# Optimization experiments

Measured on AMD Instinct MI355X. Metric: run time of the kernel, lower is better.

Reference implementation:

```python
import jax, jax.numpy as jnp
import numpy as np

B, S, D = 2, 2048, 2048
H, KVH, HD = 8, 1, 256
N_REP = H // KVH
WIN = 1024
THETA = 10000.0
SCALE = 1.0 / (HD ** 0.5)


def setup_inputs() -> dict:
    key = jax.random.key(0)
    k1, k2, k3, k4, k5 = jax.random.split(key, 5)
    hidden_states = jax.random.normal(k1, (B, S, D), dtype=jnp.float32)
    neg = jnp.finfo(jnp.float32).min
    causal = jnp.where(jnp.tril(jnp.ones((S, S), jnp.float32)) == 1.0, 0.0, neg)
    attention_mask = jnp.broadcast_to(causal[None, None], (B, 1, S, S)).copy()
    position_ids = jnp.broadcast_to(jnp.arange(S, dtype=jnp.int32)[None, :], (B, S)).copy()
    std = 0.02
    Wq = std * jax.random.normal(k2, (H * HD, D), dtype=jnp.float32)
    Wk = std * jax.random.normal(k3, (KVH * HD, D), dtype=jnp.float32)
    Wv = std * jax.random.normal(k4, (KVH * HD, D), dtype=jnp.float32)
    Wo = std * jax.random.normal(k5, (D, H * HD), dtype=jnp.float32)
    return {"hidden_states": hidden_states, "attention_mask": attention_mask,
            "position_ids": position_ids, "Wq": Wq, "Wk": Wk, "Wv": Wv, "Wo": Wo}


def _rotate_half(x):
    x1, x2 = x[..., : HD // 2], x[..., HD // 2:]
    return jnp.concatenate([-x2, x1], axis=-1)


def _rope(position_ids):
    inv_freq = 1.0 / (THETA ** (jnp.arange(0, HD, 2, dtype=jnp.float32) / HD))  # [HD/2]
    freqs = position_ids.astype(jnp.float32)[:, :, None] * inv_freq  # [b,s,HD/2]
    emb = jnp.concatenate([freqs, freqs], axis=-1)  # [b,s,HD]
    # unsqueeze at head dim -> [b,1,s,HD]
    return jnp.cos(emb)[:, None], jnp.sin(emb)[:, None]


def reference(hidden_states, attention_mask, position_ids, Wq, Wk, Wv, Wo):
    b, s, _ = hidden_states.shape
    q = (hidden_states @ Wq.T).reshape(b, s, H, HD).transpose(0, 2, 1, 3)    # [b,H,s,hd]
    k = (hidden_states @ Wk.T).reshape(b, s, KVH, HD).transpose(0, 2, 1, 3)  # [b,KVH,s,hd]
    v = (hidden_states @ Wv.T).reshape(b, s, KVH, HD).transpose(0, 2, 1, 3)

    cos, sin = _rope(position_ids)
    q = q * cos + _rotate_half(q) * sin
    k = k * cos + _rotate_half(k) * sin

    neg = jnp.finfo(attention_mask.dtype).min
    ones = jnp.ones_like(attention_mask)
    sliding = jnp.triu(ones, -(WIN - 1)) * jnp.tril(ones, WIN - 1)
    mask = jnp.where(sliding == 1.0, attention_mask, neg)  # [b,1,s,s]

    # GQA without materializing repeated KV: group query heads by kv head
    qg = q.reshape(b, KVH, N_REP, s, HD)
    scores = jnp.einsum('bgrqd,bgkd->bgrqk', qg, k) * SCALE
    scores = scores + mask[:, :, None]  # broadcast over rep dim
    probs = jax.nn.softmax(scores, axis=-1)
    out = jnp.einsum('bgrqk,bgkd->bgrqd', probs, v)  # [b,KVH,rep,s,hd]
    out = out.reshape(b, H, s, HD).transpose(0, 2, 1, 3).reshape(b, s, H * HD)
    return out @ Wo.T
```

## Files before the change

kernel.cpp:

```cpp
#include <hip/hip_runtime.h>
#include <stdint.h>

typedef __attribute__((ext_vector_type(8))) short bf16x8;
typedef __attribute__((ext_vector_type(4))) float f32x4;
typedef __attribute__((ext_vector_type(4))) unsigned short u16x4;

#define LOG2E 1.44269504088896340736f
#define SCALE 0.0625f

__device__ __forceinline__ unsigned short f32_bf16(float f) {
  unsigned int u = __float_as_uint(f);
  u += 0x7fffu + ((u >> 16) & 1u);
  return (unsigned short)(u >> 16);
}
__device__ __forceinline__ float bf16_f32(unsigned short h) {
  return __uint_as_float(((unsigned int)h) << 16);
}

__device__ __forceinline__ void gload16(const unsigned short* g, unsigned short* l) {
  __builtin_amdgcn_global_load_lds((const __attribute__((address_space(1))) void*)g,
                                   (__attribute__((address_space(3))) void*)l, 16, 0, 0);
}

__device__ __forceinline__ void cast4(const float* __restrict__ in,
                                      unsigned short* __restrict__ out, int i) {
  const float4 v = ((const float4*)in)[i];
  u16x4 o;
  o[0] = f32_bf16(v.x); o[1] = f32_bf16(v.y); o[2] = f32_bf16(v.z); o[3] = f32_bf16(v.w);
  ((u16x4*)out)[i] = o;
}

__global__ __launch_bounds__(256) void prep(const float* __restrict__ hidden,
                                            const float* __restrict__ Wq,
                                            const float* __restrict__ Wk,
                                            const float* __restrict__ Wv,
                                            const int* __restrict__ pos,
                                            unsigned short* __restrict__ hid_bf,
                                            unsigned short* __restrict__ w_bf,
                                            float* __restrict__ ctab,
                                            float* __restrict__ stab) {
  int i = blockIdx.x * 256 + threadIdx.x;
  if (i < 2097152) {
    cast4(hidden, hid_bf, i);
  } else if (i < 3145728) {
    cast4(Wq, w_bf, i - 2097152);
  } else if (i < 3276800) {
    cast4(Wk, w_bf + 4194304, i - 3145728);
  } else if (i < 3407872) {
    cast4(Wv, w_bf + 4718592, i - 3276800);
  } else {
    int j = i - 3407872;
    int d = j & 127, s = (j >> 7) & 2047, b = j >> 18;
    float p = (float)pos[b * 2048 + s];
    float f = p * exp2f(-(float)d * 0.10381025296523f);
    float sn, c;
    sincosf(f, &sn, &c);
    ctab[j] = c;
    stab[j] = sn;
  }
}

template<int OUTF32>
__global__ __launch_bounds__(256) void gemm_nt(const unsigned short* __restrict__ A,
                                               const unsigned short* __restrict__ B,
                                               void* __restrict__ Cp,
                                               int M, int N, int K) {
  __shared__ unsigned short As[2][128 * 32];
  __shared__ unsigned short Bs[2][128 * 32];
  const int t = threadIdx.x;
  const int lane = t & 63;
  const int wave = t >> 6;
  const int wr = (wave >> 1) * 64;
  const int wc = (wave & 1) * 64;
  const int l15 = lane & 15, lg = lane >> 4;

  const int gx = gridDim.x, gy = gridDim.y;
  int orig = blockIdx.y * gx + blockIdx.x;
  int nwg = gx * gy;
  int wg = orig;
  if ((nwg & 7) == 0) wg = (orig & 7) * (nwg >> 3) + (orig >> 3);
  const int bx = wg / gy, by = wg % gy;
  const long m0 = (long)by * 128;
  const long n0 = (long)bx * 128;

  f32x4 acc[4][4];
#pragma unroll
  for (int m = 0; m < 4; ++m)
#pragma unroll
    for (int n = 0; n < 4; ++n) acc[m][n] = (f32x4){0.f, 0.f, 0.f, 0.f};

  const int srow = t >> 2;
  const int scol = (t & 3) * 8;
  const unsigned short* Ag = A + (m0 + srow) * (long)K + scol;
  const unsigned short* Bg = B + (n0 + srow) * (long)K + scol;

  auto stage = [&](int buf, int k0) {
    gload16(Ag + k0, &As[buf][t * 8]);
    gload16(Ag + (long)64 * K + k0, &As[buf][2048 + t * 8]);
    gload16(Bg + k0, &Bs[buf][t * 8]);
    gload16(Bg + (long)64 * K + k0, &Bs[buf][2048 + t * 8]);
  };

  stage(0, 0);
  __syncthreads();
  int cur = 0;
  for (int k0 = 0; k0 < K; k0 += 32) {
    if (k0 + 32 < K) stage(cur ^ 1, k0 + 32);
    bf16x8 af[4], bfr[4];
#pragma unroll
    for (int m = 0; m < 4; ++m) af[m] = *(const bf16x8*)&As[cur][(wr + m * 16 + l15) * 32 + lg * 8];
#pragma unroll
    for (int n = 0; n < 4; ++n) bfr[n] = *(const bf16x8*)&Bs[cur][(wc + n * 16 + l15) * 32 + lg * 8];
    __builtin_amdgcn_s_setprio(1);
#pragma unroll
    for (int m = 0; m < 4; ++m)
#pragma unroll
      for (int n = 0; n < 4; ++n)
        acc[m][n] = __builtin_amdgcn_mfma_f32_16x16x32_bf16(af[m], bfr[n], acc[m][n], 0, 0, 0);
    __builtin_amdgcn_s_setprio(0);
    __syncthreads();
    cur ^= 1;
  }

#pragma unroll
  for (int m = 0; m < 4; ++m)
#pragma unroll
    for (int n = 0; n < 4; ++n)
#pragma unroll
      for (int r = 0; r < 4; ++r) {
        long row = m0 + wr + m * 16 + lg * 4 + r;
        long col = n0 + wc + n * 16 + l15;
        if (OUTF32)
          ((float*)Cp)[row * N + col] = acc[m][n][r];
        else
          ((unsigned short*)Cp)[row * N + col] = f32_bf16(acc[m][n][r]);
      }
}

__global__ __launch_bounds__(256) void mid(unsigned short* __restrict__ qkv,
                                           const float* __restrict__ ctab,
                                           const float* __restrict__ stab,
                                           unsigned short* __restrict__ vt,
                                           const float* __restrict__ Wo,
                                           unsigned short* __restrict__ wo_bf) {
  __shared__ unsigned short tile[64][68];
  const int bi = blockIdx.x, t = threadIdx.x;
  if (bi < 2304) {
    int i = bi * 256 + t;
    int g = i & 15;
    int hh = (i >> 4) % 9;
    int sb_ = (i >> 4) / 9;
    int s = sb_ & 2047, b = sb_ >> 11;
    size_t base = (size_t)(b * 2048 + s) * 2560 + (hh == 8 ? 2048 : hh * 256) + g * 8;
    const float* ct = ctab + ((size_t)(b * 2048 + s) << 7) + g * 8;
    const float* st = stab + ((size_t)(b * 2048 + s) << 7) + g * 8;
    const float sc = (hh == 8) ? 1.0f : SCALE;
    bf16x8 lo = *(const bf16x8*)(qkv + base);
    bf16x8 hi = *(const bf16x8*)(qkv + base + 128);
    bf16x8 lo2, hi2;
#pragma unroll
    for (int e = 0; e < 8; ++e) {
      float c = ct[e] * sc, sn = st[e] * sc;
      float x1 = bf16_f32((unsigned short)lo[e]);
      float x2 = bf16_f32((unsigned short)hi[e]);
      lo2[e] = (short)f32_bf16(x1 * c - x2 * sn);
      hi2[e] = (short)f32_bf16(x2 * c + x1 * sn);
    }
    *(bf16x8*)(qkv + base) = lo2;
    *(bf16x8*)(qkv + base + 128) = hi2;
  } else if (bi < 2560) {
    int bb = bi - 2304;
    const int s0 = (bb & 31) * 64, d0 = ((bb >> 5) & 3) * 64, b = bb >> 7;
    const int r = t >> 4, c4 = (t & 15) * 4;
#pragma unroll
    for (int j = 0; j < 4; ++j) {
      int row = r + j * 16;
      const unsigned short* src = qkv + (size_t)(b * 2048 + s0 + row) * 2560 + 2304 + d0 + c4;
#pragma unroll
      for (int e = 0; e < 4; ++e) tile[row][c4 + e] = src[e];
    }
    __syncthreads();
#pragma unroll
    for (int j = 0; j < 4; ++j) {
      int drow = r + j * 16;
      u16x4 o;
#pragma unroll
      for (int e = 0; e < 4; ++e) o[e] = tile[c4 + e][drow];
      *(u16x4*)(vt + (size_t)(b * 256 + d0 + drow) * 2048 + s0 + c4) = o;
    }
  } else {
    int i = (bi - 2560) * 256 + t;
    cast4(Wo, wo_bf, i);
  }
}

__global__ __launch_bounds__(256, 2) void attn3(const unsigned short* __restrict__ qkv,
                                                const unsigned short* __restrict__ vt,
                                                unsigned short* __restrict__ O) {
  __shared__ __align__(16) unsigned short Ks[2][32 * 256];
  const int t = threadIdx.x, lane = t & 63, wave = t >> 6;
  const int l15 = lane & 15, lg = lane >> 4;
  const int qb = blockIdx.x, h = blockIdx.y, b = blockIdx.z;
  const int q0 = qb * 64;
  const int qw = q0 + wave * 16;
  const int qg = qw + l15;

  bf16x8 qf[8];
  {
    const unsigned short* qp = qkv + (size_t)(b * 2048 + qg) * 2560 + h * 256 + lg * 8;
#pragma unroll
    for (int c = 0; c < 8; ++c) qf[c] = *(const bf16x8*)(qp + c * 32);
  }

  size_t kgb[4];
  int klo[4];
#pragma unroll
  for (int p = 0; p < 4; ++p) {
    int i = p * 256 + t;
    int kr = i >> 5, kb = (i & 31) << 4;
    int ksrc = kb ^ ((kr & 7) << 4);
    kgb[p] = (size_t)(b * 2048 + kr) * 2560 + 2048 + (ksrc >> 1);
    klo[p] = i * 8;
  }

  const unsigned short* vbase = vt + (size_t)b * 524288 + (size_t)l15 * 2048 + lg * 8;

  f32x4 oacc[16];
#pragma unroll
  for (int dt = 0; dt < 16; ++dt) oacc[dt] = (f32x4){0.f, 0.f, 0.f, 0.f};
  float mrun = -3e30f, lrun = 0.f;

  int ks0 = q0 - 1023;
  if (ks0 < 0) ks0 = 0;
  ks0 &= ~31;
  const int nst = (q0 + 64 - ks0) >> 5;

#pragma unroll
  for (int p = 0; p < 4; ++p) gload16(qkv + kgb[p] + (size_t)ks0 * 2560, &Ks[0][klo[p]]);
  __syncthreads();

  for (int si = 0; si < nst; ++si) {
    const int ks = ks0 + si * 32;
    const int cur = si & 1;
    if (si + 1 < nst) {
      const size_t ko = (size_t)(ks + 32) * 2560;
#pragma unroll
      for (int p = 0; p < 4; ++p) gload16(qkv + kgb[p] + ko, &Ks[cur ^ 1][klo[p]]);
    }

    const bool live = !((ks > qw + 15) || (ks + 31 <= qw - 1024));
    if (live) {
      bf16x8 vf[16];
#pragma unroll
      for (int dt = 0; dt < 16; ++dt)
        vf[dt] = *(const bf16x8*)(vbase + (size_t)dt * 32768 + ks);

      const unsigned short* Kc = Ks[cur];
      f32x4 sa = (f32x4){0.f, 0.f, 0.f, 0.f};
      f32x4 sb2 = (f32x4){0.f, 0.f, 0.f, 0.f};
      const int kswz = (l15 & 7) << 4;
      __builtin_amdgcn_s_setprio(1);
#pragma unroll
      for (int c = 0; c < 8; ++c) {
        const int off = ((c * 64 + lg * 16) ^ kswz) >> 1;
        bf16x8 k0 = *(const bf16x8*)&Kc[l15 * 256 + off];
        bf16x8 k1 = *(const bf16x8*)&Kc[(16 + l15) * 256 + off];
        sa = __builtin_amdgcn_mfma_f32_16x16x32_bf16(k0, qf[c], sa, 0, 0, 0);
        sb2 = __builtin_amdgcn_mfma_f32_16x16x32_bf16(k1, qf[c], sb2, 0, 0, 0);
      }
      __builtin_amdgcn_s_setprio(0);

      float pv[8];
      const bool full = (ks + 31 <= qw) && (ks > qw - 1009);
      if (full) {
#pragma unroll
        for (int r = 0; r < 4; ++r) { pv[r] = sa[r]; pv[4 + r] = sb2[r]; }
      } else {
        const int kb0 = ks + lg * 4, kb1 = kb0 + 16;
        const int lo_b = qg - 1024;
#pragma unroll
        for (int r = 0; r < 4; ++r) {
          int k0i = kb0 + r, k1i = kb1 + r;
          pv[r] = (k0i <= qg && k0i > lo_b) ? sa[r] : -3e38f;
          pv[4 + r] = (k1i <= qg && k1i > lo_b) ? sb2[r] : -3e38f;
        }
      }
      float mx = fmaxf(fmaxf(fmaxf(pv[0], pv[1]), fmaxf(pv[2], pv[3])),
                       fmaxf(fmaxf(pv[4], pv[5]), fmaxf(pv[6], pv[7])));
      mx = fmaxf(mx, __shfl_xor(mx, 16));
      mx = fmaxf(mx, __shfl_xor(mx, 32));
      if (!__all(mx - mrun <= 8.0f)) {
        float mnew = fmaxf(mrun, mx);
        float al = exp2f((mrun - mnew) * LOG2E);
#pragma unroll
        for (int dt = 0; dt < 16; ++dt) oacc[dt] *= al;
        lrun *= al;
        mrun = mnew;
      }
      float ps = 0.f;
#pragma unroll
      for (int j = 0; j < 8; ++j) {
        pv[j] = exp2f((pv[j] - mrun) * LOG2E);
        ps += pv[j];
      }
      ps += __shfl_xor(ps, 16);
      ps += __shfl_xor(ps, 32);
      lrun += ps;

      unsigned int w0 = ((unsigned int)f32_bf16(pv[1]) << 16) | f32_bf16(pv[0]);
      unsigned int w1 = ((unsigned int)f32_bf16(pv[3]) << 16) | f32_bf16(pv[2]);
      unsigned int w2 = ((unsigned int)f32_bf16(pv[5]) << 16) | f32_bf16(pv[4]);
      unsigned int w3 = ((unsigned int)f32_bf16(pv[7]) << 16) | f32_bf16(pv[6]);
      unsigned int sA0 = (lg < 2) ? w2 : w0;
      unsigned int sA1 = (lg < 2) ? w3 : w1;
      unsigned int rA0 = (unsigned int)__shfl_xor((int)sA0, 32);
      unsigned int rA1 = (unsigned int)__shfl_xor((int)sA1, 32);
      unsigned int own0 = (lg < 2) ? w0 : w2;
      unsigned int own1 = (lg < 2) ? w1 : w3;
      const bool sendOwn = ((lg ^ (lg >> 1)) & 1) != 0;
      unsigned int sB0 = sendOwn ? own0 : rA0;
      unsigned int sB1 = sendOwn ? own1 : rA1;
      unsigned int rB0 = (unsigned int)__shfl_xor((int)sB0, 16);
      unsigned int rB1 = (unsigned int)__shfl_xor((int)sB1, 16);
      union { unsigned int u[4]; bf16x8 v; } pu;
      pu.u[0] = (lg == 0) ? own0 : ((lg == 2) ? rA0 : rB0);
      pu.u[1] = (lg == 0) ? own1 : ((lg == 2) ? rA1 : rB1);
      pu.u[2] = (lg == 3) ? own0 : ((lg == 1) ? rA0 : rB0);
      pu.u[3] = (lg == 3) ? own1 : ((lg == 1) ? rA1 : rB1);

      __builtin_amdgcn_s_setprio(1);
#pragma unroll
      for (int dt = 0; dt < 16; ++dt)
        oacc[dt] = __builtin_amdgcn_mfma_f32_16x16x32_bf16(vf[dt], pu.v, oacc[dt], 0, 0, 0);
      __builtin_amdgcn_s_setprio(0);
    }
    __syncthreads();
  }

  float inv = 1.0f / lrun;
  unsigned short* op = O + (size_t)(b * 2048 + qg) * 2048 + h * 256 + lg * 4;
#pragma unroll
  for (int dt = 0; dt < 16; ++dt) {
    u16x4 o4;
#pragma unroll
    for (int r = 0; r < 4; ++r) o4[r] = f32_bf16(oacc[dt][r] * inv);
    *(u16x4*)(op + dt * 16) = o4;
  }
}

extern "C" void kernel_launch(void* const* d_in, const int* in_sizes, int n_in,
                              void* d_out, int out_size, void* d_ws, size_t ws_size,
                              hipStream_t stream) {
  const float* hidden = (const float*)d_in[0];
  const int* pos_ids = (const int*)d_in[2];
  const float* Wq = (const float*)d_in[3];
  const float* Wk = (const float*)d_in[4];
  const float* Wv = (const float*)d_in[5];
  const float* Wo = (const float*)d_in[6];
  float* out = (float*)d_out;
  char* ws = (char*)d_ws;

  unsigned short* qkv_bf = (unsigned short*)(ws);
  unsigned short* hid_bf = (unsigned short*)(ws + 20971520);
  unsigned short* w_bf   = (unsigned short*)(ws + 37748736);
  unsigned short* vtbuf  = (unsigned short*)(ws + 48234496);
  float*          ctab   = (float*)(ws + 50331648);
  float*          stab   = (float*)(ws + 52428800);
  unsigned short* attno  = hid_bf;

  prep<<<15360, 256, 0, stream>>>(hidden, Wq, Wk, Wv, pos_ids, hid_bf, w_bf, ctab, stab);

  gemm_nt<0><<<dim3(20, 32), 256, 0, stream>>>(hid_bf, w_bf, qkv_bf, 4096, 2560, 2048);

  mid<<<6656, 256, 0, stream>>>(qkv_bf, ctab, stab, vtbuf, Wo, w_bf);

  attn3<<<dim3(32, 8, 2), 256, 0, stream>>>(qkv_bf, vtbuf, attno);

  gemm_nt<1><<<dim3(16, 32), 256, 0, stream>>>(attno, w_bf, out, 4096, 2048, 2048);
}
```

Baseline: 384.5 us.

## Stage V tiles through swizzled LDS with register prefetch in attention kernel

The attention kernel used to have every wave load its V fragments straight from global memory, so the four waves in a block fetched the same V tile redundantly. Now the block loads V cooperatively into a swizzled shared-memory tile. The next tile is prefetched into registers and written to LDS after an extra barrier. Occupancy bounds go from 2 to 3 blocks per CU to make up for the lower register pressure. In exchange there is a second __syncthreads per iteration and extra LDS traffic, and if the register limit forces spills the occupancy gain could be lost.

```diff
diff --git a/kernel.cpp b/kernel.cpp
--- a/kernel.cpp
+++ b/kernel.cpp
@@ -194,10 +194,11 @@
   }
 }
 
-__global__ __launch_bounds__(256, 2) void attn3(const unsigned short* __restrict__ qkv,
+__global__ __launch_bounds__(256, 3) void attn4(const unsigned short* __restrict__ qkv,
                                                 const unsigned short* __restrict__ vt,
                                                 unsigned short* __restrict__ O) {
   __shared__ __align__(16) unsigned short Ks[2][32 * 256];
+  __shared__ __align__(16) unsigned short Vs[256 * 32];
   const int t = threadIdx.x, lane = t & 63, wave = t >> 6;
   const int l15 = lane & 15, lg = lane >> 4;
   const int qb = blockIdx.x, h = blockIdx.y, b = blockIdx.z;
@@ -212,8 +213,8 @@
     for (int c = 0; c < 8; ++c) qf[c] = *(const bf16x8*)(qp + c * 32);
   }
 
-  size_t kgb[4];
-  int klo[4];
+  size_t kgb[4], vgb[4];
+  int klo[4], vlo[4];
 #pragma unroll
   for (int p = 0; p < 4; ++p) {
     int i = p * 256 + t;
@@ -221,9 +222,11 @@
     int ksrc = kb ^ ((kr & 7) << 4);
     kgb[p] = (size_t)(b * 2048 + kr) * 2560 + 2048 + (ksrc >> 1);
     klo[p] = i * 8;
-  }
-
-  const unsigned short* vbase = vt + (size_t)b * 524288 + (size_t)l15 * 2048 + lg * 8;
+    int vr = i >> 2, vb = (i & 3) << 4;
+    int vsrc = vb ^ (((vr >> 1) & 3) << 4);
+    vgb[p] = (size_t)(b * 256 + vr) * 2048 + (vsrc >> 1);
+    vlo[p] = i * 8;
+  }
 
   f32x4 oacc[16];
 #pragma unroll
@@ -237,24 +240,25 @@
 
 #pragma unroll
   for (int p = 0; p < 4; ++p) gload16(qkv + kgb[p] + (size_t)ks0 * 2560, &Ks[0][klo[p]]);
+#pragma unroll
+  for (int p = 0; p < 4; ++p) gload16(vt + vgb[p] + ks0, &Vs[vlo[p]]);
   __syncthreads();
 
   for (int si = 0; si < nst; ++si) {
     const int ks = ks0 + si * 32;
     const int cur = si & 1;
-    if (si + 1 < nst) {
+    const bool havenext = (si + 1 < nst);
+    bf16x8 vst[4];
+    if (havenext) {
       const size_t ko = (size_t)(ks + 32) * 2560;
 #pragma unroll
       for (int p = 0; p < 4; ++p) gload16(qkv + kgb[p] + ko, &Ks[cur ^ 1][klo[p]]);
+#pragma unroll
+      for (int p = 0; p < 4; ++p) vst[p] = *(const bf16x8*)(vt + vgb[p] + (ks + 32));
     }
 
     const bool live = !((ks > qw + 15) || (ks + 31 <= qw - 1024));
     if (live) {
-      bf16x8 vf[16];
-#pragma unroll
-      for (int dt = 0; dt < 16; ++dt)
-        vf[dt] = *(const bf16x8*)(vbase + (size_t)dt * 32768 + ks);
-
       const unsigned short* Kc = Ks[cur];
       f32x4 sa = (f32x4){0.f, 0.f, 0.f, 0.f};
       f32x4 sb2 = (f32x4){0.f, 0.f, 0.f, 0.f};
@@ -328,11 +332,19 @@
       pu.u[2] = (lg == 3) ? own0 : ((lg == 1) ? rA0 : rB0);
       pu.u[3] = (lg == 3) ? own1 : ((lg == 1) ? rA1 : rB1);
 
+      const int vswz = (lg * 16) ^ (((l15 >> 1) & 3) << 4);
       __builtin_amdgcn_s_setprio(1);
 #pragma unroll
-      for (int dt = 0; dt < 16; ++dt)
-        oacc[dt] = __builtin_amdgcn_mfma_f32_16x16x32_bf16(vf[dt], pu.v, oacc[dt], 0, 0, 0);
+      for (int dt = 0; dt < 16; ++dt) {
+        bf16x8 vf = *(const bf16x8*)&Vs[(dt * 16 + l15) * 32 + (vswz >> 1)];
+        oacc[dt] = __builtin_amdgcn_mfma_f32_16x16x32_bf16(vf, pu.v, oacc[dt], 0, 0, 0);
+      }
       __builtin_amdgcn_s_setprio(0);
+    }
+    __syncthreads();
+    if (havenext) {
+#pragma unroll
+      for (int p = 0; p < 4; ++p) *(bf16x8*)&Vs[vlo[p]] = vst[p];
     }
     __syncthreads();
   }
@@ -374,7 +386,7 @@
 
   mid<<<6656, 256, 0, stream>>>(qkv_bf, ctab, stab, vtbuf, Wo, w_bf);
 
-  attn3<<<dim3(32, 8, 2), 256, 0, stream>>>(qkv_bf, vtbuf, attno);
+  attn4<<<dim3(32, 8, 2), 256, 0, stream>>>(qkv_bf, vtbuf, attno);
 
   gemm_nt<1><<<dim3(16, 32), 256, 0, stream>>>(attno, w_bf, out, 4096, 2048, 2048);
 }
```

Result: faster. 351.7 us (-8.5%).
